# Performance work log

Measured on AMD Instinct MI355X. Metric: run time of the kernel, lower is better.

## Reference

```python
import jax, jax.numpy as jnp
import numpy as np
from jax import lax

NPOINT = 1024
RADIUS = 0.2
NSAMPLE = 32
MLP = (64, 64, 128)
BN_EPS = 1e-3  # keras BatchNormalization default epsilon


def setup_inputs() -> dict:
    key = jax.random.key(0)
    ks = jax.random.split(key, 8)
    B, N, C = 8, 8192, 64
    d = {
        'xyz': jax.random.uniform(ks[0], (B, N, 3), jnp.float32),
        'points': jax.random.normal(ks[1], (B, N, C), jnp.float32),
    }
    cin = C + 3  # use_xyz=True concatenates relative xyz
    for li, f in enumerate(MLP):
        d[f'w{li}'] = jax.random.normal(ks[2 + li], (cin, f), jnp.float32) * (1.0 / np.sqrt(cin))
        d[f'gamma{li}'] = jnp.ones((f,), jnp.float32)
        d[f'beta{li}'] = jnp.zeros((f,), jnp.float32)
        cin = f
    return d


def _fps(xyz, npoint):
    """Farthest point sampling. xyz: (B,N,3) -> (B,npoint) int32."""
    B, N, _ = xyz.shape

    def body(carry, _):
        dist, far = carry
        centroid = jnp.take_along_axis(xyz, far[:, None, None], axis=1)  # (B,1,3)
        d = jnp.sum((xyz - centroid) ** 2, axis=-1)  # (B,N)
        dist = jnp.minimum(dist, d)
        nxt = jnp.argmax(dist, axis=-1).astype(jnp.int32)
        return (dist, nxt), far

    init = (jnp.full((B, N), 1e10, xyz.dtype), jnp.zeros((B,), jnp.int32))
    _, idx = lax.scan(body, init, None, length=npoint)
    return jnp.transpose(idx)  # (B, npoint)


def _ball_query(xyz, new_xyz, radius, nsample):
    """xyz: (B,N,3), new_xyz: (B,S,3) -> (B,S,nsample) int32 neighbor idx."""
    B, S, _ = new_xyz.shape
    N = xyz.shape[1]
    sqr = jnp.sum((new_xyz[:, :, None, :] - xyz[:, None, :, :]) ** 2, axis=-1)  # (B,S,N)
    idx = jnp.broadcast_to(jnp.arange(N, dtype=jnp.int32), (B, S, N))
    idx = jnp.where(sqr > radius * radius, N, idx)
    idx = jnp.sort(idx, axis=-1)[:, :, :nsample]
    first = idx[:, :, :1]  # center itself is always in-radius -> valid
    return jnp.where(idx == N, first, idx)


def _gather(x, idx):
    """x: (B,N,C), idx: (B,S,K) -> (B,S,K,C)."""
    B, S, K = idx.shape
    flat = jnp.take_along_axis(x, idx.reshape(B, S * K)[:, :, None], axis=1)
    return flat.reshape(B, S, K, x.shape[-1])


def _bn_relu(x, gamma, beta):
    # training-mode batchnorm over (batch, npoint, nsample) axes
    m = jnp.mean(x, axis=(0, 1, 2), keepdims=True)
    v = jnp.var(x, axis=(0, 1, 2), keepdims=True)
    return jax.nn.relu(gamma * (x - m) * lax.rsqrt(v + BN_EPS) + beta)


def reference(xyz, points, w0, gamma0, beta0, w1, gamma1, beta1, w2, gamma2, beta2):
    fps_idx = _fps(xyz, NPOINT)  # (B,S)
    new_xyz = jnp.take_along_axis(xyz, fps_idx[:, :, None], axis=1)  # (B,S,3)
    idx = _ball_query(xyz, new_xyz, RADIUS, NSAMPLE)  # (B,S,K)
    grouped_xyz = _gather(xyz, idx) - new_xyz[:, :, None, :]  # (B,S,K,3)
    grouped_pts = _gather(points, idx)  # (B,S,K,C)
    x = jnp.concatenate([grouped_xyz, grouped_pts], axis=-1)  # (B,S,K,3+C)
    for w, g, b in ((w0, gamma0, beta0), (w1, gamma1, beta1), (w2, gamma2, beta2)):
        x = _bn_relu(jnp.einsum('bskc,cf->bskf', x, w), g, b)
    new_points = jnp.max(x, axis=2)  # (B,S,F) == squeeze of keepdims max
    return new_xyz, new_points
```

## Files before the change

kernel.cpp:

```cpp
#include <hip/hip_runtime.h>
#include <hip/hip_bf16.h>
#include <stdint.h>


#define INV_CNT (1.0f/262144.0f)

typedef __attribute__((ext_vector_type(8))) short bf16x8;
typedef __attribute__((ext_vector_type(4))) float f32x4;
typedef __attribute__((ext_vector_type(2))) float f32x2;

__device__ __forceinline__ float bf2f(unsigned int v) {
    return __uint_as_float(v << 16);
}
__device__ __forceinline__ unsigned int f2bf(float f) {
    unsigned int u = __float_as_uint(f);
    return (u + 0x7fffu + ((u >> 16) & 1u)) >> 16;
}

template<int CTRL>
__device__ __forceinline__ unsigned int dpp_u32(unsigned int x) {
    return (unsigned int)__builtin_amdgcn_update_dpp((int)x, (int)x, CTRL, 0xf, 0xf, false);
}
template<int CTRL>
__device__ __forceinline__ float dpp_f32(float x) {
    return __uint_as_float(dpp_u32<CTRL>(__float_as_uint(x)));
}

__global__ __launch_bounds__(256) void fps_kernel(const float* __restrict__ xyz,
                                                  float* __restrict__ nxyz,
                                                  float* __restrict__ out_nxyz) {
#pragma clang fp contract(off)
    const int b = blockIdx.x;
    const int t = threadIdx.x;
    const int lane = t & 63;
    const int wv = t >> 6;
    const float* xb = xyz + (size_t)b * 8192 * 3;
    __shared__ float4 sxyz[8192];
    __shared__ unsigned long long sdk[2][4];
    __shared__ int ch[1024];
    f32x2 px[16], py[16], pz[16], dist[16];
#pragma unroll
    for (int j = 0; j < 16; ++j) {
        int p0 = t + (2*j)*256, p1 = t + (2*j+1)*256;
        float x0 = xb[p0*3+0], y0 = xb[p0*3+1], z0 = xb[p0*3+2];
        float x1 = xb[p1*3+0], y1 = xb[p1*3+1], z1 = xb[p1*3+2];
        px[j] = (f32x2){x0, x1}; py[j] = (f32x2){y0, y1}; pz[j] = (f32x2){z0, z1};
        sxyz[p0] = make_float4(x0, y0, z0, 0.f);
        sxyz[p1] = make_float4(x1, y1, z1, 0.f);
        dist[j] = (f32x2){1e10f, 1e10f};
    }
    __syncthreads();
    int far = 0;
    for (int it = 0; it < 1024; ++it) {
        if (t == 0) ch[it] = far;
        float4 c4 = sxyz[far];
        f32x2 c2x = (f32x2){c4.x, c4.x}, c2y = (f32x2){c4.y, c4.y}, c2z = (f32x2){c4.z, c4.z};
        float bv0 = -1.f, bv1 = -1.f;
#pragma unroll
        for (int j = 0; j < 16; ++j) {
            f32x2 dx = px[j] - c2x;
            f32x2 dy = py[j] - c2y;
            f32x2 dz = pz[j] - c2z;
            f32x2 dd = (dx*dx + dy*dy) + dz*dz;
            float n0 = fminf(dist[j][0], dd[0]);
            float n1 = fminf(dist[j][1], dd[1]);
            dist[j][0] = n0; dist[j][1] = n1;
            bv0 = fmaxf(bv0, n0); bv1 = fmaxf(bv1, n1);
        }
        float bestv = fmaxf(bv0, bv1);
        unsigned int cand[32];
#pragma unroll
        for (int j = 0; j < 16; ++j) {
            cand[2*j]   = (dist[j][0] == bestv) ? (unsigned int)(2*j)   : 64u;
            cand[2*j+1] = (dist[j][1] == bestv) ? (unsigned int)(2*j+1) : 64u;
        }
#pragma unroll
        for (int s = 16; s >= 1; s >>= 1)
#pragma unroll
            for (int i = 0; i < s; ++i) cand[i] = (cand[i+s] < cand[i]) ? cand[i+s] : cand[i];
        float v = bestv;
        v = fmaxf(v, dpp_f32<0x111>(v));
        v = fmaxf(v, dpp_f32<0x112>(v));
        v = fmaxf(v, dpp_f32<0x114>(v));
        v = fmaxf(v, dpp_f32<0x118>(v));
        v = fmaxf(v, dpp_f32<0x142>(v));
        v = fmaxf(v, dpp_f32<0x143>(v));
        unsigned int wmu = (unsigned int)__builtin_amdgcn_readlane((int)__float_as_uint(v), 63);
        float wm = __uint_as_float(wmu);
        unsigned int idx = (unsigned int)t + (cand[0] << 8);
        if (bestv != wm) idx = 0xffffffffu;
        { unsigned int n;
          n = dpp_u32<0x111>(idx); idx = (n < idx) ? n : idx;
          n = dpp_u32<0x112>(idx); idx = (n < idx) ? n : idx;
          n = dpp_u32<0x114>(idx); idx = (n < idx) ? n : idx;
          n = dpp_u32<0x118>(idx); idx = (n < idx) ? n : idx;
          n = dpp_u32<0x142>(idx); idx = (n < idx) ? n : idx;
          n = dpp_u32<0x143>(idx); idx = (n < idx) ? n : idx; }
        if (lane == 63)
            sdk[it & 1][wv] = ((unsigned long long)wmu << 32) | (unsigned long long)(~idx);
        __syncthreads();
        unsigned long long k = sdk[it & 1][lane & 3];
        unsigned int xh = (unsigned int)(k >> 32), xl = (unsigned int)k;
#define XSTEP(C) { unsigned int nh = dpp_u32<C>(xh), nl = dpp_u32<C>(xl);          \
                   unsigned long long nk = ((unsigned long long)nh << 32) | nl;     \
                   unsigned long long ck = ((unsigned long long)xh << 32) | xl;     \
                   bool tk = nk > ck; xh = tk ? nh : xh; xl = tk ? nl : xl; }
        XSTEP(0x111) XSTEP(0x112)
#undef XSTEP
        far = (int)(~(unsigned int)__builtin_amdgcn_readlane((int)xl, 3)) & 8191;
    }
    __syncthreads();
    for (int j = t; j < 1024; j += 256) {
        float4 c4 = sxyz[ch[j]];
        size_t o = (size_t)(b*1024 + j) * 3;
        nxyz[o] = c4.x; nxyz[o+1] = c4.y; nxyz[o+2] = c4.z;
        out_nxyz[o] = c4.x; out_nxyz[o+1] = c4.y; out_nxyz[o+2] = c4.z;
    }
}

__global__ __launch_bounds__(256) void ballquery_kernel(const float* __restrict__ xyz,
                                                        const float* __restrict__ nxyz,
                                                        int* __restrict__ idxbuf) {
    const int wib = threadIdx.x >> 6;
    const int lane = threadIdx.x & 63;
    const int c = blockIdx.x * 4 + wib;
    const int b = c >> 10;
    const float* xb = xyz + (size_t)b * 8192 * 3;
    const float cx = nxyz[c*3+0], cy = nxyz[c*3+1], cz = nxyz[c*3+2];
    const float R2 = 0.04f;
    int count = 0, first = 0;
    int* ob = idxbuf + (size_t)c * 32;
    for (int base = 0; base < 8192; base += 64) {
        int i = base + lane;
        float dx = __fsub_rn(xb[i*3+0], cx);
        float dy = __fsub_rn(xb[i*3+1], cy);
        float dz = __fsub_rn(xb[i*3+2], cz);
        float sq = __fadd_rn(__fadd_rn(__fmul_rn(dx,dx), __fmul_rn(dy,dy)), __fmul_rn(dz,dz));
        bool pass = !(sq > R2);
        unsigned long long mask = __ballot(pass);
        if (count == 0 && mask) first = base + (int)__builtin_ctzll(mask);
        int pos = count + (int)__popcll(mask & ((1ull << lane) - 1ull));
        if (pass && pos < 32) ob[pos] = i;
        count += (int)__popcll(mask);
        if (count >= 32) break;
    }
    if (count < 32 && lane >= count && lane < 32) ob[lane] = first;
}

__global__ __launch_bounds__(256) void prep_w(const float* __restrict__ w0,
                                              const float* __restrict__ w1,
                                              const float* __restrict__ w2,
                                              unsigned short* __restrict__ wt0,
                                              unsigned short* __restrict__ wt1,
                                              unsigned short* __restrict__ wt2) {
    const int i0 = blockIdx.x * 256 + threadIdx.x;
    const int stride = gridDim.x * 256;
    for (int i = i0; i < 64*104; i += stride) {
        int f = i / 104, k = i - f*104;
        wt0[i] = (k < 67) ? (unsigned short)f2bf(w0[k*64 + f]) : (unsigned short)0;
    }
    for (int i = i0; i < 64*72; i += stride) {
        int f = i / 72, k = i - f*72;
        wt1[i] = (k < 64) ? (unsigned short)f2bf(w1[k*64 + f]) : (unsigned short)0;
    }
    for (int i = i0; i < 128*72; i += stride) {
        int f = i / 72, k = i - f*72;
        wt2[i] = (k < 64) ? (unsigned short)f2bf(w2[k*128 + f]) : (unsigned short)0;
    }
}


__global__ __launch_bounds__(256) void layer0_kernel(
        const float* __restrict__ xyz, const float* __restrict__ points,
        const float* __restrict__ nxyz, const int* __restrict__ idxbuf,
        const unsigned short* __restrict__ wt0, unsigned short* __restrict__ z0,
        float* __restrict__ stats0) {
    __shared__ __attribute__((aligned(16))) unsigned short Xb[64*104];
    __shared__ __attribute__((aligned(16))) unsigned short Wt[64*104];
    __shared__ float ssum[64], ssq[64];
    const int tid = threadIdx.x;
    const int R = blockIdx.x * 64;
    if (tid < 64) { ssum[tid] = 0.f; ssq[tid] = 0.f; }
    {
        const uint4* src = (const uint4*)wt0;
        uint4* dst = (uint4*)Wt;
        for (int i = tid; i < 64*104/8; i += 256) dst[i] = src[i];
    }
    {
        int r = tid >> 2, q = tid & 3;
        int row = R + r;
        int gi = idxbuf[row];
        int b = row >> 15, s = (row >> 5) & 1023;
        const float4* pb4 = (const float4*)(points + (size_t)(b*8192 + gi) * 64);
        float4 f0 = pb4[q*4+0], f1 = pb4[q*4+1], f2 = pb4[q*4+2], f3 = pb4[q*4+3];
        unsigned short* xr = &Xb[r*104 + 3 + q*16];
        xr[0]  = (unsigned short)f2bf(f0.x); xr[1]  = (unsigned short)f2bf(f0.y);
        xr[2]  = (unsigned short)f2bf(f0.z); xr[3]  = (unsigned short)f2bf(f0.w);
        xr[4]  = (unsigned short)f2bf(f1.x); xr[5]  = (unsigned short)f2bf(f1.y);
        xr[6]  = (unsigned short)f2bf(f1.z); xr[7]  = (unsigned short)f2bf(f1.w);
        xr[8]  = (unsigned short)f2bf(f2.x); xr[9]  = (unsigned short)f2bf(f2.y);
        xr[10] = (unsigned short)f2bf(f2.z); xr[11] = (unsigned short)f2bf(f2.w);
        xr[12] = (unsigned short)f2bf(f3.x); xr[13] = (unsigned short)f2bf(f3.y);
        xr[14] = (unsigned short)f2bf(f3.z); xr[15] = (unsigned short)f2bf(f3.w);
        if (q == 0) {
#pragma unroll
            for (int e = 0; e < 3; ++e) {
                float vv = xyz[(size_t)(b*8192+gi)*3 + e] - nxyz[(size_t)(b*1024+s)*3 + e];
                Xb[r*104 + e] = (unsigned short)f2bf(vv);
            }
        }
    }
    for (int i = tid; i < 29*64; i += 256) {
        int e = 67 + (i % 29), r = i / 29;
        Xb[r*104 + e] = 0;
    }
    __syncthreads();
    const int l = tid & 63, w = tid >> 6;
    const int rsub = l & 15, kq = l >> 4;
    f32x4 acc[4];
#pragma unroll
    for (int cb = 0; cb < 4; ++cb) acc[cb] = (f32x4){0.f, 0.f, 0.f, 0.f};
    const int abase = (w*16 + rsub)*104 + kq*8;
    const int bbase = rsub*104 + kq*8;
#pragma unroll
    for (int ks = 0; ks < 3; ++ks) {
        bf16x8 A = *(const bf16x8*)&Xb[abase + ks*32];
#pragma unroll
        for (int cb = 0; cb < 4; ++cb) {
            bf16x8 Bf = *(const bf16x8*)&Wt[bbase + cb*16*104 + ks*32];
            acc[cb] = __builtin_amdgcn_mfma_f32_16x16x32_bf16(A, Bf, acc[cb], 0, 0, 0);
        }
    }
    unsigned short* zrow = z0 + (size_t)(R + w*16 + kq*4) * 64;
#pragma unroll
    for (int cb = 0; cb < 4; ++cb) {
        int c = cb*16 + rsub;
        float a0 = acc[cb][0], a1 = acc[cb][1], a2 = acc[cb][2], a3 = acc[cb][3];
        atomicAdd(&ssum[c], a0 + a1 + a2 + a3);
        atomicAdd(&ssq[c], a0*a0 + a1*a1 + a2*a2 + a3*a3);
#pragma unroll
        for (int j = 0; j < 4; ++j) zrow[j*64 + c] = (unsigned short)f2bf(acc[cb][j]);
    }
    __syncthreads();
    if (tid < 64) {
        atomicAdd(&stats0[tid], ssum[tid]);
        atomicAdd(&stats0[64+tid], ssq[tid]);
    }
}

__global__ __launch_bounds__(256) void layer1_kernel(
        const unsigned short* __restrict__ z0, const float* __restrict__ stats0,
        const float* __restrict__ gamma0, const float* __restrict__ beta0,
        const unsigned short* __restrict__ wt1, unsigned short* __restrict__ z1,
        float* __restrict__ stats1) {
    __shared__ __attribute__((aligned(16))) unsigned short Xb[64*72];
    __shared__ __attribute__((aligned(16))) unsigned short Wt[64*72];
    __shared__ float scale[64], shift[64], ssum[64], ssq[64];
    const int tid = threadIdx.x;
    const int R = blockIdx.x * 64;
    if (tid < 64) {
        float m = stats0[tid] * INV_CNT;
        float v = stats0[64+tid] * INV_CNT - m*m;
        float rs = rsqrtf(v + 1e-3f);
        float sc = gamma0[tid] * rs;
        scale[tid] = sc; shift[tid] = beta0[tid] - m*sc;
        ssum[tid] = 0.f; ssq[tid] = 0.f;
    }
    {
        const uint4* src = (const uint4*)wt1;
        uint4* dst = (uint4*)Wt;
        for (int i = tid; i < 64*72/8; i += 256) dst[i] = src[i];
    }
    __syncthreads();
    const uint4* zg = (const uint4*)(z0 + (size_t)R * 64);
#pragma unroll
    for (int cch = 0; cch < 2; ++cch) {
        int flat8 = tid*2 + cch;
        uint4 a = zg[flat8];
        int r = flat8 >> 3, e0 = (flat8 & 7) * 8;
        unsigned int uu[4] = {a.x, a.y, a.z, a.w};
        bf16x8 xv;
#pragma unroll
        for (int j = 0; j < 8; ++j) {
            unsigned int ub = (j & 1) ? (uu[j>>1] >> 16) : (uu[j>>1] & 0xffffu);
            float v = bf2f(ub);
            v = fmaxf(v * scale[e0+j] + shift[e0+j], 0.f);
            xv[j] = (short)f2bf(v);
        }
        *(bf16x8*)&Xb[r*72 + e0] = xv;
    }
    __syncthreads();
    const int l = tid & 63, w = tid >> 6;
    const int rsub = l & 15, kq = l >> 4;
    f32x4 acc[4];
#pragma unroll
    for (int cb = 0; cb < 4; ++cb) acc[cb] = (f32x4){0.f, 0.f, 0.f, 0.f};
    const int abase = (w*16 + rsub)*72 + kq*8;
    const int bbase = rsub*72 + kq*8;
#pragma unroll
    for (int ks = 0; ks < 2; ++ks) {
        bf16x8 A = *(const bf16x8*)&Xb[abase + ks*32];
#pragma unroll
        for (int cb = 0; cb < 4; ++cb) {
            bf16x8 Bf = *(const bf16x8*)&Wt[bbase + cb*16*72 + ks*32];
            acc[cb] = __builtin_amdgcn_mfma_f32_16x16x32_bf16(A, Bf, acc[cb], 0, 0, 0);
        }
    }
    unsigned short* zrow = z1 + (size_t)(R + w*16 + kq*4) * 64;
#pragma unroll
    for (int cb = 0; cb < 4; ++cb) {
        int c = cb*16 + rsub;
        float a0 = acc[cb][0], a1 = acc[cb][1], a2 = acc[cb][2], a3 = acc[cb][3];
        atomicAdd(&ssum[c], a0 + a1 + a2 + a3);
        atomicAdd(&ssq[c], a0*a0 + a1*a1 + a2*a2 + a3*a3);
#pragma unroll
        for (int j = 0; j < 4; ++j) zrow[j*64 + c] = (unsigned short)f2bf(acc[cb][j]);
    }
    __syncthreads();
    if (tid < 64) {
        atomicAdd(&stats1[tid], ssum[tid]);
        atomicAdd(&stats1[64+tid], ssq[tid]);
    }
}

__global__ __launch_bounds__(256) void layer2_kernel(
        const unsigned short* __restrict__ z1, const float* __restrict__ stats1,
        const float* __restrict__ gamma1, const float* __restrict__ beta1,
        const unsigned short* __restrict__ wt2, float* __restrict__ maxz2,
        float* __restrict__ stats2) {
    __shared__ __attribute__((aligned(16))) unsigned short Xb[64*72];
    __shared__ __attribute__((aligned(16))) unsigned short Wt[128*72];
    __shared__ float scale[64], shift[64];
    __shared__ float ssum[128], ssq[128];
    __shared__ float gmx[2][8][128];
    const int tid = threadIdx.x;
    const int R = blockIdx.x * 64;
    if (tid < 64) {
        float m = stats1[tid] * INV_CNT;
        float v = stats1[64+tid] * INV_CNT - m*m;
        float rs = rsqrtf(v + 1e-3f);
        float sc = gamma1[tid] * rs;
        scale[tid] = sc; shift[tid] = beta1[tid] - m*sc;
    }
    if (tid < 128) { ssum[tid] = 0.f; ssq[tid] = 0.f; }
    {
        const uint4* src = (const uint4*)wt2;
        uint4* dst = (uint4*)Wt;
        for (int i = tid; i < 128*72/8; i += 256) dst[i] = src[i];
    }
    __syncthreads();
    const uint4* zg = (const uint4*)(z1 + (size_t)R * 64);
#pragma unroll
    for (int cch = 0; cch < 2; ++cch) {
        int flat8 = tid*2 + cch;
        uint4 a = zg[flat8];
        int r = flat8 >> 3, e0 = (flat8 & 7) * 8;
        unsigned int uu[4] = {a.x, a.y, a.z, a.w};
        bf16x8 xv;
#pragma unroll
        for (int j = 0; j < 8; ++j) {
            unsigned int ub = (j & 1) ? (uu[j>>1] >> 16) : (uu[j>>1] & 0xffffu);
            float v = bf2f(ub);
            v = fmaxf(v * scale[e0+j] + shift[e0+j], 0.f);
            xv[j] = (short)f2bf(v);
        }
        *(bf16x8*)&Xb[r*72 + e0] = xv;
    }
    __syncthreads();
    const int l = tid & 63, w = tid >> 6;
    const int rsub = l & 15, kq = l >> 4;
    f32x4 acc[8];
#pragma unroll
    for (int cb = 0; cb < 8; ++cb) acc[cb] = (f32x4){0.f, 0.f, 0.f, 0.f};
    const int abase = (w*16 + rsub)*72 + kq*8;
    const int bbase = rsub*72 + kq*8;
#pragma unroll
    for (int ks = 0; ks < 2; ++ks) {
        bf16x8 A = *(const bf16x8*)&Xb[abase + ks*32];
#pragma unroll
        for (int cb = 0; cb < 8; ++cb) {
            bf16x8 Bf = *(const bf16x8*)&Wt[bbase + cb*16*72 + ks*32];
            acc[cb] = __builtin_amdgcn_mfma_f32_16x16x32_bf16(A, Bf, acc[cb], 0, 0, 0);
        }
    }
    const int g = w >> 1;
    const int contrib = (w & 1) * 4 + kq;
#pragma unroll
    for (int cb = 0; cb < 8; ++cb) {
        int c = cb*16 + rsub;
        float a0 = acc[cb][0], a1 = acc[cb][1], a2 = acc[cb][2], a3 = acc[cb][3];
        atomicAdd(&ssum[c], a0 + a1 + a2 + a3);
        atomicAdd(&ssq[c], a0*a0 + a1*a1 + a2*a2 + a3*a3);
        gmx[g][contrib][c] = fmaxf(fmaxf(a0, a1), fmaxf(a2, a3));
    }
    __syncthreads();
    {
        int gg = tid >> 7, c = tid & 127;
        float m = gmx[gg][0][c];
#pragma unroll
        for (int i = 1; i < 8; ++i) m = fmaxf(m, gmx[gg][i][c]);
        maxz2[(size_t)(blockIdx.x*2 + gg) * 128 + c] = m;
    }
    if (tid < 128) {
        atomicAdd(&stats2[tid], ssum[tid]);
        atomicAdd(&stats2[128+tid], ssq[tid]);
    }
}

__global__ __launch_bounds__(256) void final_kernel(
        const float* __restrict__ maxz2, const float* __restrict__ stats2,
        const float* __restrict__ gamma2, const float* __restrict__ beta2,
        float* __restrict__ out) {
    const int i = blockIdx.x * 256 + threadIdx.x;
    const int f = i & 127;
    float m = stats2[f] * INV_CNT;
    float v = stats2[128+f] * INV_CNT - m*m;
    float rs = rsqrtf(v + 1e-3f);
    out[24576 + i] = fmaxf(gamma2[f]*((maxz2[i]-m)*rs) + beta2[f], 0.f);
}

extern "C" void kernel_launch(void* const* d_in, const int* in_sizes, int n_in,
                              void* d_out, int out_size, void* d_ws, size_t ws_size,
                              hipStream_t stream) {
    const float* xyz    = (const float*)d_in[0];
    const float* points = (const float*)d_in[1];
    const float* w0     = (const float*)d_in[2];
    const float* g0     = (const float*)d_in[3];
    const float* b0     = (const float*)d_in[4];
    const float* w1     = (const float*)d_in[5];
    const float* g1     = (const float*)d_in[6];
    const float* b1     = (const float*)d_in[7];
    const float* w2     = (const float*)d_in[8];
    const float* g2     = (const float*)d_in[9];
    const float* b2     = (const float*)d_in[10];
    float* out = (float*)d_out;
    char* ws = (char*)d_ws;

    float* nxyz            = (float*)(ws + 0);
    int*   idxbuf          = (int*)  (ws + 98304);
    float* stats           = (float*)(ws + 1146880);
    unsigned short* z0     = (unsigned short*)(ws + 1148928);
    unsigned short* z1     = (unsigned short*)(ws + 34703360);
    float* maxz2           = (float*)(ws + 68257792);
    unsigned short* wt0    = (unsigned short*)(ws + 72452096);
    unsigned short* wt1    = (unsigned short*)(ws + 72465408);
    unsigned short* wt2    = (unsigned short*)(ws + 72474624);

    hipMemsetAsync(stats, 0, 512 * sizeof(float), stream);
    prep_w<<<26, 256, 0, stream>>>(w0, w1, w2, wt0, wt1, wt2);
    fps_kernel<<<8, 256, 0, stream>>>(xyz, nxyz, out);
    ballquery_kernel<<<2048, 256, 0, stream>>>(xyz, nxyz, idxbuf);
    layer0_kernel<<<4096, 256, 0, stream>>>(xyz, points, nxyz, idxbuf, wt0, z0, stats);
    layer1_kernel<<<4096, 256, 0, stream>>>(z0, stats, g0, b0, wt1, z1, stats + 128);
    layer2_kernel<<<4096, 256, 0, stream>>>(z1, stats + 128, g1, b1, wt2, maxz2, stats + 256);
    final_kernel<<<4096, 256, 0, stream>>>(maxz2, stats + 256, g2, b2, out);
}
```

Measured before the change: 1.363 ms.

## Spread BN stat atomics over 32 banks, precompute scale/shift, rebalance FPS max tree

Global BatchNorm sum and sum-of-squares atomics are spread over 32 per-block-index banks to cut same-address contention across 4096 blocks. Tiny prep kernels then reduce the banks and precompute per-channel scale and shift, so the layer kernels and the final kernel no longer redo the rsqrt math per block or per element. The FPS loop splits the min-update from the max-reduction and uses a shallower max tree to shorten the dependency chain. This adds three small kernel launches and a larger memset.

```diff
diff --git a/kernel.cpp b/kernel.cpp
--- a/kernel.cpp
+++ b/kernel.cpp
@@ -55,19 +55,26 @@
         if (t == 0) ch[it] = far;
         float4 c4 = sxyz[far];
         f32x2 c2x = (f32x2){c4.x, c4.x}, c2y = (f32x2){c4.y, c4.y}, c2z = (f32x2){c4.z, c4.z};
-        float bv0 = -1.f, bv1 = -1.f;
 #pragma unroll
         for (int j = 0; j < 16; ++j) {
             f32x2 dx = px[j] - c2x;
             f32x2 dy = py[j] - c2y;
             f32x2 dz = pz[j] - c2z;
             f32x2 dd = (dx*dx + dy*dy) + dz*dz;
-            float n0 = fminf(dist[j][0], dd[0]);
-            float n1 = fminf(dist[j][1], dd[1]);
-            dist[j][0] = n0; dist[j][1] = n1;
-            bv0 = fmaxf(bv0, n0); bv1 = fmaxf(bv1, n1);
-        }
-        float bestv = fmaxf(bv0, bv1);
+            dist[j][0] = fminf(dist[j][0], dd[0]);
+            dist[j][1] = fminf(dist[j][1], dd[1]);
+        }
+        float tm[16];
+#pragma unroll
+        for (int j = 0; j < 16; ++j) tm[j] = fmaxf(dist[j][0], dist[j][1]);
+        float g0 = fmaxf(fmaxf(tm[0], tm[1]), tm[2]);
+        float g1 = fmaxf(fmaxf(tm[3], tm[4]), tm[5]);
+        float g2 = fmaxf(fmaxf(tm[6], tm[7]), tm[8]);
+        float g3 = fmaxf(fmaxf(tm[9], tm[10]), tm[11]);
+        float g4 = fmaxf(fmaxf(tm[12], tm[13]), tm[14]);
+        float h0 = fmaxf(fmaxf(g0, g1), g2);
+        float h1 = fmaxf(fmaxf(g3, g4), tm[15]);
+        float bestv = fmaxf(h0, h1);
         unsigned int cand[32];
 #pragma unroll
         for (int j = 0; j < 16; ++j) {
@@ -169,6 +176,31 @@
     }
 }
 
+__global__ void bnprep64(const float* __restrict__ st,
+                         const float* __restrict__ gamma, const float* __restrict__ beta,
+                         float* __restrict__ sc, float* __restrict__ sh) {
+    const int c = threadIdx.x;
+    float s = 0.f, q = 0.f;
+    for (int b = 0; b < 32; ++b) { s += st[b*128 + c]; q += st[b*128 + 64 + c]; }
+    float m = s * INV_CNT;
+    float v = q * INV_CNT - m*m;
+    float rs = rsqrtf(v + 1e-3f);
+    float scl = gamma[c] * rs;
+    sc[c] = scl; sh[c] = beta[c] - m*scl;
+}
+__global__ void bnprep128(const float* __restrict__ st,
+                          const float* __restrict__ gamma, const float* __restrict__ beta,
+                          float* __restrict__ sc, float* __restrict__ sh) {
+    const int c = threadIdx.x;
+    float s = 0.f, q = 0.f;
+    for (int b = 0; b < 32; ++b) { s += st[b*256 + c]; q += st[b*256 + 128 + c]; }
+    float m = s * INV_CNT;
+    float v = q * INV_CNT - m*m;
+    float rs = rsqrtf(v + 1e-3f);
+    float scl = gamma[c] * rs;
+    sc[c] = scl; sh[c] = beta[c] - m*scl;
+}
+
 
 __global__ __launch_bounds__(256) void layer0_kernel(
         const float* __restrict__ xyz, const float* __restrict__ points,
@@ -180,6 +212,7 @@
     __shared__ float ssum[64], ssq[64];
     const int tid = threadIdx.x;
     const int R = blockIdx.x * 64;
+    const int bank = blockIdx.x & 31;
     if (tid < 64) { ssum[tid] = 0.f; ssq[tid] = 0.f; }
     {
         const uint4* src = (const uint4*)wt0;
@@ -243,14 +276,14 @@
     }
     __syncthreads();
     if (tid < 64) {
-        atomicAdd(&stats0[tid], ssum[tid]);
-        atomicAdd(&stats0[64+tid], ssq[tid]);
+        atomicAdd(&stats0[bank*128 + tid], ssum[tid]);
+        atomicAdd(&stats0[bank*128 + 64 + tid], ssq[tid]);
     }
 }
 
 __global__ __launch_bounds__(256) void layer1_kernel(
-        const unsigned short* __restrict__ z0, const float* __restrict__ stats0,
-        const float* __restrict__ gamma0, const float* __restrict__ beta0,
+        const unsigned short* __restrict__ z0,
+        const float* __restrict__ gsc, const float* __restrict__ gsh,
         const unsigned short* __restrict__ wt1, unsigned short* __restrict__ z1,
         float* __restrict__ stats1) {
     __shared__ __attribute__((aligned(16))) unsigned short Xb[64*72];
@@ -258,12 +291,9 @@
     __shared__ float scale[64], shift[64], ssum[64], ssq[64];
     const int tid = threadIdx.x;
     const int R = blockIdx.x * 64;
+    const int bank = blockIdx.x & 31;
     if (tid < 64) {
-        float m = stats0[tid] * INV_CNT;
-        float v = stats0[64+tid] * INV_CNT - m*m;
-        float rs = rsqrtf(v + 1e-3f);
-        float sc = gamma0[tid] * rs;
-        scale[tid] = sc; shift[tid] = beta0[tid] - m*sc;
+        scale[tid] = gsc[tid]; shift[tid] = gsh[tid];
         ssum[tid] = 0.f; ssq[tid] = 0.f;
     }
     {
@@ -318,14 +348,14 @@
     }
     __syncthreads();
     if (tid < 64) {
-        atomicAdd(&stats1[tid], ssum[tid]);
-        atomicAdd(&stats1[64+tid], ssq[tid]);
+        atomicAdd(&stats1[bank*128 + tid], ssum[tid]);
+        atomicAdd(&stats1[bank*128 + 64 + tid], ssq[tid]);
     }
 }
 
 __global__ __launch_bounds__(256) void layer2_kernel(
-        const unsigned short* __restrict__ z1, const float* __restrict__ stats1,
-        const float* __restrict__ gamma1, const float* __restrict__ beta1,
+        const unsigned short* __restrict__ z1,
+        const float* __restrict__ gsc, const float* __restrict__ gsh,
         const unsigned short* __restrict__ wt2, float* __restrict__ maxz2,
         float* __restrict__ stats2) {
     __shared__ __attribute__((aligned(16))) unsigned short Xb[64*72];
@@ -335,13 +365,8 @@
     __shared__ float gmx[2][8][128];
     const int tid = threadIdx.x;
     const int R = blockIdx.x * 64;
-    if (tid < 64) {
-        float m = stats1[tid] * INV_CNT;
-        float v = stats1[64+tid] * INV_CNT - m*m;
-        float rs = rsqrtf(v + 1e-3f);
-        float sc = gamma1[tid] * rs;
-        scale[tid] = sc; shift[tid] = beta1[tid] - m*sc;
-    }
+    const int bank = blockIdx.x & 31;
+    if (tid < 64) { scale[tid] = gsc[tid]; shift[tid] = gsh[tid]; }
     if (tid < 128) { ssum[tid] = 0.f; ssq[tid] = 0.f; }
     {
         const uint4* src = (const uint4*)wt2;
@@ -402,21 +427,18 @@
         maxz2[(size_t)(blockIdx.x*2 + gg) * 128 + c] = m;
     }
     if (tid < 128) {
-        atomicAdd(&stats2[tid], ssum[tid]);
-        atomicAdd(&stats2[128+tid], ssq[tid]);
+        atomicAdd(&stats2[bank*256 + tid], ssum[tid]);
+        atomicAdd(&stats2[bank*256 + 128 + tid], ssq[tid]);
     }
 }
 
 __global__ __launch_bounds__(256) void final_kernel(
-        const float* __restrict__ maxz2, const float* __restrict__ stats2,
-        const float* __restrict__ gamma2, const float* __restrict__ beta2,
+        const float* __restrict__ maxz2,
+        const float* __restrict__ sc, const float* __restrict__ sh,
         float* __restrict__ out) {
     const int i = blockIdx.x * 256 + threadIdx.x;
     const int f = i & 127;
-    float m = stats2[f] * INV_CNT;
-    float v = stats2[128+f] * INV_CNT - m*m;
-    float rs = rsqrtf(v + 1e-3f);
-    out[24576 + i] = fmaxf(gamma2[f]*((maxz2[i]-m)*rs) + beta2[f], 0.f);
+    out[24576 + i] = fmaxf(maxz2[i]*sc[f] + sh[f], 0.f);
 }
 
 extern "C" void kernel_launch(void* const* d_in, const int* in_sizes, int n_in,
@@ -438,20 +460,30 @@
 
     float* nxyz            = (float*)(ws + 0);
     int*   idxbuf          = (int*)  (ws + 98304);
-    float* stats           = (float*)(ws + 1146880);
     unsigned short* z0     = (unsigned short*)(ws + 1148928);
     unsigned short* z1     = (unsigned short*)(ws + 34703360);
     float* maxz2           = (float*)(ws + 68257792);
     unsigned short* wt0    = (unsigned short*)(ws + 72452096);
     unsigned short* wt1    = (unsigned short*)(ws + 72465408);
     unsigned short* wt2    = (unsigned short*)(ws + 72474624);
-
-    hipMemsetAsync(stats, 0, 512 * sizeof(float), stream);
+    float* statsB          = (float*)(ws + 72493056);
+    float* st0             = statsB;
+    float* st1             = statsB + 4096;
+    float* st2             = statsB + 8192;
+    float* scsh            = (float*)(ws + 72558592);
+    float* sc0 = scsh,        * sh0 = scsh + 64;
+    float* sc1 = scsh + 128,  * sh1 = scsh + 192;
+    float* sc2 = scsh + 256,  * sh2 = scsh + 384;
+
+    hipMemsetAsync(statsB, 0, 16384 * sizeof(float), stream);
     prep_w<<<26, 256, 0, stream>>>(w0, w1, w2, wt0, wt1, wt2);
     fps_kernel<<<8, 256, 0, stream>>>(xyz, nxyz, out);
     ballquery_kernel<<<2048, 256, 0, stream>>>(xyz, nxyz, idxbuf);
-    layer0_kernel<<<4096, 256, 0, stream>>>(xyz, points, nxyz, idxbuf, wt0, z0, stats);
-    layer1_kernel<<<4096, 256, 0, stream>>>(z0, stats, g0, b0, wt1, z1, stats + 128);
-    layer2_kernel<<<4096, 256, 0, stream>>>(z1, stats + 128, g1, b1, wt2, maxz2, stats + 256);
-    final_kernel<<<4096, 256, 0, stream>>>(maxz2, stats + 256, g2, b2, out);
-}
+    layer0_kernel<<<4096, 256, 0, stream>>>(xyz, points, nxyz, idxbuf, wt0, z0, st0);
+    bnprep64<<<1, 64, 0, stream>>>(st0, g0, b0, sc0, sh0);
+    layer1_kernel<<<4096, 256, 0, stream>>>(z0, sc0, sh0, wt1, z1, st1);
+    bnprep64<<<1, 64, 0, stream>>>(st1, g1, b1, sc1, sh1);
+    layer2_kernel<<<4096, 256, 0, stream>>>(z1, sc1, sh1, wt2, maxz2, st2);
+    bnprep128<<<1, 128, 0, stream>>>(st2, g2, b2, sc2, sh2);
+    final_kernel<<<4096, 256, 0, stream>>>(maxz2, sc2, sh2, out);
+}
```

Result: faster. 1.249 ms (-8.3%).
